# Performance work log

Measured on AMD Instinct MI355X. Metric: run time of the kernel, lower is better.

## Reference

```python
import jax, jax.numpy as jnp
import numpy as np

B, N, C, H, W = 2, 512, 32, 200, 200
THRESH = 0.05
# BEVCamera: x_range=y_range=(-1,1) -> FoV=2 meters; sh = H/FoVy = 100, sw = W/FoVx = 100
SH = H / 2.0
SW = W / 2.0
LOWPASS = 0.3        # 3DGS low-pass filter added to 2D cov diagonal
ALPHA_MIN = 1.0 / 255.0
ALPHA_MAX = 0.99


def setup_inputs() -> dict:
    key = jax.random.key(0)
    k1, k2, k3, k4 = jax.random.split(key, 4)
    features = jax.random.normal(k1, (B, N, C), dtype=jnp.float32)
    means3D = jax.random.uniform(k2, (B, N, 3), dtype=jnp.float32, minval=-1.0, maxval=1.0)
    # build PSD 3D covariances: Sigma = A A^T + eps*I, store 6 upper-tri entries
    A = 0.05 * jax.random.normal(k3, (B, N, 3, 3), dtype=jnp.float32)
    S = jnp.einsum('bnij,bnkj->bnik', A, A) + 1e-4 * jnp.eye(3, dtype=jnp.float32)
    cov3D = jnp.stack([S[..., 0, 0], S[..., 0, 1], S[..., 0, 2],
                       S[..., 1, 1], S[..., 1, 2], S[..., 2, 2]], axis=-1)
    opacities = jax.random.uniform(k4, (B, N, 1), dtype=jnp.float32)
    return {"features": features, "means3D": means3D, "cov3D": cov3D, "opacities": opacities}


def _render_one(features, means3D, cov3D, op):
    # features [N,C], means3D [N,3], cov3D [N,6] (xx,xy,xz,yy,yz,zz), op [N,1]
    dtype = features.dtype
    opac = op[:, 0]
    opac = jnp.where(opac > THRESH, opac, 0.0)  # masked-out gaussians contribute nothing
    # projmatrix: u = H/2 - sh*y (height), v = W/2 - sw*x (width)
    mu_u = H / 2.0 - SH * means3D[:, 1]
    mu_v = W / 2.0 - SW * means3D[:, 0]
    # 2D covariance from orthographic BEV projection J = [[0,-sh,0],[-sw,0,0]]
    Cuu = SH * SH * cov3D[:, 3] + LOWPASS
    Cvv = SW * SW * cov3D[:, 0] + LOWPASS
    Cuv = SH * SW * cov3D[:, 1]
    det = Cuu * Cvv - Cuv * Cuv
    valid = det > 0.0
    inv_det = jnp.where(valid, 1.0 / jnp.where(valid, det, 1.0), 0.0)
    Iuu = Cvv * inv_det
    Ivv = Cuu * inv_det
    Iuv = -Cuv * inv_det
    opac = jnp.where(valid, opac, 0.0)
    uu = jnp.arange(H, dtype=dtype)
    vv = jnp.arange(W, dtype=dtype)
    du = uu[None, :, None] - mu_u[:, None, None]   # [N,H,1]
    dv = vv[None, None, :] - mu_v[:, None, None]   # [N,1,W]
    power = (-0.5 * (Iuu[:, None, None] * du * du + Ivv[:, None, None] * dv * dv)
             - Iuv[:, None, None] * du * dv)       # [N,H,W]
    alpha = jnp.minimum(ALPHA_MAX, opac[:, None, None] * jnp.exp(jnp.minimum(power, 0.0)))
    alpha = jnp.where((power > 0.0) | (alpha < ALPHA_MIN), 0.0, alpha)
    # front-to-back alpha compositing in gaussian index order (all depths are 0 -> stable sort)
    logt = jnp.log1p(-alpha)                       # [N,H,W]
    T = jnp.exp(jnp.cumsum(logt, axis=0) - logt)   # exclusive transmittance
    w = T * alpha                                  # [N,H,W]
    return jnp.einsum('nhw,nc->chw', w, features)  # bg color is zeros


def reference(features, means3D, cov3D, opacities):
    bev = jax.vmap(_render_one)(features, means3D, cov3D, opacities)  # [B,C,H,W]
    num_gaussians = (opacities[..., 0] > THRESH).astype(jnp.float32).sum(axis=-1).mean()
    return bev, num_gaussians
```

## Files before the change

kernel.cpp:

```cpp
#include <hip/hip_runtime.h>
#include <math.h>

#define B_ 2
#define N_ 512
#define C_ 32
#define H_ 200
#define W_ 200
#define HW_ (H_*W_)
#define THRESH_ 0.05f
#define OUT_BEV (B_*C_*H_*W_)
#define NSEG 4
#define TILES_PER_B 625
#define LOG2E 1.4426950408889634f
#define LN2   0.6931471805599453f

typedef float v2f __attribute__((ext_vector_type(2)));

__device__ __forceinline__ float rlane(float x, int l) {
    return __int_as_float(__builtin_amdgcn_readlane(__float_as_int(x), l));
}

__device__ __forceinline__ void pcompute(
    const float* __restrict__ m3, const float* __restrict__ cv,
    const float* __restrict__ opc, int i,
    float& mu_u, float& mu_v, float& a2, float& b2, float& c2,
    float& opo, float& thr2, float& inv2a, float& inv2b)
{
    float x  = m3[i*3 + 0];
    float y  = m3[i*3 + 1];
    float c0 = cv[i*6 + 0];
    float c1 = cv[i*6 + 1];
    float c3 = cv[i*6 + 3];
    float op = opc[i];
    mu_u = 100.0f - 100.0f * y;
    mu_v = 100.0f - 100.0f * x;
    float Cuu = 10000.0f * c3 + 0.3f;
    float Cvv = 10000.0f * c0 + 0.3f;
    float Cuv = 10000.0f * c1;
    float det = Cuu * Cvv - Cuv * Cuv;
    bool valid = det > 0.0f;
    float opac = (op > THRESH_) ? op : 0.0f;
    if (!valid) opac = 0.0f;
    float inv_det = valid ? (1.0f / det) : 0.0f;
    a2 = -0.5f * LOG2E * (Cvv * inv_det);
    b2 = -0.5f * LOG2E * (Cuu * inv_det);
    c2 =  LOG2E * (Cuv * inv_det);
    opo = opac;
    if (opac > 0.0f) {
        thr2 = -log2f(255.0f * opac);
        inv2a = 1.0f / (2.0f * a2);
        inv2b = 1.0f / (2.0f * b2);
    } else {
        thr2 = 3.0e38f;
        inv2a = 0.0f;
        inv2b = 0.0f;
    }
}

__device__ __forceinline__ float edge_max_u(float a2, float b2, float c2,
                                            float due, float dvlo, float dvhi,
                                            float inv2b) {
    float dvs = fminf(fmaxf(-c2 * due * inv2b, dvlo), dvhi);
    return fmaf(a2 * due, due, fmaf(b2 * dvs, dvs, c2 * (due * dvs)));
}
__device__ __forceinline__ float edge_max_v(float a2, float b2, float c2,
                                            float dve, float dulo, float duhi,
                                            float inv2a) {
    float dus = fminf(fmaxf(-c2 * dve * inv2a, dulo), duhi);
    return fmaf(a2 * dus, dus, fmaf(b2 * dve, dve, c2 * (dus * dve)));
}

#define OVTEST(P, ovname)                                                     \
    bool ovname;                                                              \
    {                                                                         \
        float dulo = tu0 - P##_mu_u, duhi = tu1 - P##_mu_u;                   \
        float dvlo = tv0 - P##_mu_v, dvhi = tv1 - P##_mu_v;                   \
        bool inside = (dulo <= 0.0f) & (duhi >= 0.0f) &                       \
                      (dvlo <= 0.0f) & (dvhi >= 0.0f);                        \
        float e0 = edge_max_u(P##_a, P##_b, P##_c, dulo, dvlo, dvhi, P##_i2b);\
        float e1 = edge_max_u(P##_a, P##_b, P##_c, duhi, dvlo, dvhi, P##_i2b);\
        float e2 = edge_max_v(P##_a, P##_b, P##_c, dvlo, dulo, duhi, P##_i2a);\
        float e3 = edge_max_v(P##_a, P##_b, P##_c, dvhi, dulo, duhi, P##_i2a);\
        float mx = fmaxf(fmaxf(e0, e1), fmaxf(e2, e3));                       \
        ovname = (P##_op > 0.0f) && (inside || (mx >= P##_th));               \
    }

#define WALK(mask, P, base_n)                                                \
    while (mask) {                                                           \
        int j0 = __builtin_ctzll(mask); mask &= mask - 1;                    \
        bool two = (mask != 0ull);                                           \
        int j1 = two ? __builtin_ctzll(mask) : j0;                           \
        if (two) mask &= mask - 1;                                           \
        float mu_u0 = rlane(P##_mu_u, j0), mu_v0 = rlane(P##_mu_v, j0);      \
        float a0 = rlane(P##_a, j0), b0 = rlane(P##_b, j0);                  \
        float c0 = rlane(P##_c, j0), op0 = rlane(P##_op, j0);                \
        float th0 = rlane(P##_th, j0);                                       \
        float mu_u1 = rlane(P##_mu_u, j1), mu_v1 = rlane(P##_mu_v, j1);      \
        float a1 = rlane(P##_a, j1), b1 = rlane(P##_b, j1);                  \
        float c1 = rlane(P##_c, j1), op1 = rlane(P##_op, j1);                \
        float th1 = rlane(P##_th, j1);                                       \
        const v2f* f0 = (const v2f*)(featB + (size_t)((base_n) + j0) * C_);  \
        const v2f* f1 = (const v2f*)(featB + (size_t)((base_n) + j1) * C_);  \
        float du0 = u - mu_u0, dv0 = v - mu_v0;                              \
        float pw0 = fmaf(a0 * du0, du0, fmaf(b0 * dv0, dv0, c0 * (du0 * dv0))); \
        bool hit0 = (pw0 <= 0.0f) && (pw0 >= th0);                           \
        float al0 = hit0 ? fminf(0.99f, op0 * exp2f(pw0)) : 0.0f;            \
        float du1 = u - mu_u1, dv1 = v - mu_v1;                              \
        float pw1 = fmaf(a1 * du1, du1, fmaf(b1 * dv1, dv1, c1 * (du1 * dv1))); \
        bool hit1 = two && (pw1 <= 0.0f) && (pw1 >= th1);                    \
        float al1 = hit1 ? fminf(0.99f, op1 * exp2f(pw1)) : 0.0f;            \
        if (__any(hit0 | hit1)) {                                            \
            float w0 = T * al0;                                              \
            float Tm = T * (1.0f - al0);                                     \
            float w1 = Tm * al1;                                             \
            T = Tm * (1.0f - al1);                                           \
            v2f w0v = {w0, w0}, w1v = {w1, w1};                              \
            _Pragma("unroll")                                                \
            for (int i = 0; i < 16; ++i)                                     \
                acc2[i] = __builtin_elementwise_fma(w1v, f1[i],              \
                          __builtin_elementwise_fma(w0v, f0[i], acc2[i]));   \
        }                                                                    \
    }

__global__ __launch_bounds__(256, 5) void render_kernel(
    const float* __restrict__ features,
    const float* __restrict__ means3D,
    const float* __restrict__ cov3D,
    const float* __restrict__ opacities,
    float* __restrict__ out)
{
    __shared__ float s_T[NSEG][64];
    __shared__ unsigned int s_pk[NSEG * 16 * 64];

    int blk = blockIdx.x;
    int tid = threadIdx.x;

    if (blk == B_ * TILES_PER_B) {
        int cnt = ((opacities[tid]       > THRESH_) ? 1 : 0)
                + ((opacities[tid + 256] > THRESH_) ? 1 : 0)
                + ((opacities[tid + 512] > THRESH_) ? 1 : 0)
                + ((opacities[tid + 768] > THRESH_) ? 1 : 0);
        for (int off = 32; off > 0; off >>= 1) cnt += __shfl_down(cnt, off);
        int* s_red = (int*)s_T;
        if ((tid & 63) == 0) s_red[tid >> 6] = cnt;
        __syncthreads();
        if (tid == 0)
            out[OUT_BEV] = (float)(s_red[0] + s_red[1] + s_red[2] + s_red[3]) * 0.5f;
        return;
    }

    int b = blk & 1;
    int i = blk >> 1;
    int s = (int)sqrtf((float)i);
    int r = (s + 1) >> 1;
    int tu, tv;
    if (r == 0) {
        tu = 12; tv = 12;
    } else {
        int base = (2 * r - 1) * (2 * r - 1);
        int p  = i - base;
        int tr = 2 * r;
        int side = p / tr;
        int off  = p - side * tr;
        if      (side == 0) { tu = 12 - r + off; tv = 12 - r; }
        else if (side == 1) { tu = 12 + r;       tv = 12 - r + off; }
        else if (side == 2) { tu = 12 + r - off; tv = 12 + r; }
        else                { tu = 12 - r;       tv = 12 + r - off; }
    }

    int wave = __builtin_amdgcn_readfirstlane(tid >> 6);
    int lane = tid & 63;

    float tu0 = (float)(tu * 8), tu1 = tu0 + 7.0f;
    float tv0 = (float)(tv * 8), tv1 = tv0 + 7.0f;

    float A_mu_u, A_mu_v, A_a, A_b, A_c, A_op, A_th, A_i2a, A_i2b;
    float B_mu_u, B_mu_v, B_a, B_b, B_c, B_op, B_th, B_i2a, B_i2b;
    int i0 = b * N_ + wave * 128 + lane;
    pcompute(means3D, cov3D, opacities, i0,
             A_mu_u, A_mu_v, A_a, A_b, A_c, A_op, A_th, A_i2a, A_i2b);
    pcompute(means3D, cov3D, opacities, i0 + 64,
             B_mu_u, B_mu_v, B_a, B_b, B_c, B_op, B_th, B_i2a, B_i2b);

    OVTEST(A, ovA)
    OVTEST(B, ovB)
    unsigned long long m0 = __ballot(ovA);
    unsigned long long m1 = __ballot(ovB);

    int uu = tu * 8 + (lane >> 3);
    int vv = tv * 8 + (lane & 7);
    float u = (float)uu, v = (float)vv;

    float T = 1.0f;
    v2f acc2[16];
#pragma unroll
    for (int i2 = 0; i2 < 16; ++i2) acc2[i2] = (v2f){0.0f, 0.0f};
    const float* featB = features + (size_t)b * (N_ * C_);

    WALK(m0, A, wave * 128)
    WALK(m1, B, wave * 128 + 64)

    s_T[wave][lane] = T;
#pragma unroll
    for (int i2 = 0; i2 < 16; ++i2) {
        unsigned int rr;
        asm("v_cvt_pk_bf16_f32 %0, %1, %2"
            : "=v"(rr) : "v"(acc2[i2].x), "v"(acc2[i2].y));
        s_pk[(wave * 16 + i2) * 64 + lane] = rr;
    }
    __syncthreads();

    float t0g = s_T[0][lane], t1g = s_T[1][lane], t2g = s_T[2][lane];
    float Wg[NSEG];
    Wg[0] = 1.0f;
    Wg[1] = t0g;
    Wg[2] = t0g * t1g;
    Wg[3] = Wg[2] * t2g;

    size_t obase = (size_t)b * C_ * HW_ + (size_t)(tu * 8) * W_ + (size_t)(tv * 8);
    size_t opix  = (size_t)(lane >> 3) * W_ + (lane & 7);
#pragma unroll
    for (int q = 0; q < 4; ++q) {
        int pr = wave * 4 + q;
        float vlo = 0.0f, vhi = 0.0f;
#pragma unroll
        for (int g = 0; g < NSEG; ++g) {
            unsigned int rr = s_pk[(g * 16 + pr) * 64 + lane];
            float flo = __uint_as_float(rr << 16);
            float fhi = __uint_as_float(rr & 0xffff0000u);
            vlo = fmaf(Wg[g], flo, vlo);
            vhi = fmaf(Wg[g], fhi, vhi);
        }
        out[obase + (size_t)(2 * pr)     * HW_ + opix] = vlo;
        out[obase + (size_t)(2 * pr + 1) * HW_ + opix] = vhi;
    }
}

extern "C" void kernel_launch(void* const* d_in, const int* in_sizes, int n_in,
                              void* d_out, int out_size, void* d_ws, size_t ws_size,
                              hipStream_t stream) {
    const float* features  = (const float*)d_in[0];
    const float* means3D   = (const float*)d_in[1];
    const float* cov3D     = (const float*)d_in[2];
    const float* opacities = (const float*)d_in[3];
    float* out = (float*)d_out;
    render_kernel<<<B_ * TILES_PER_B + 1, 256, 0, stream>>>(
        features, means3D, cov3D, opacities, out);
}
```

Baseline: 16.50 us.

## Walk both 64-gaussian halves in parallel with independent transmittance chains

Replaces the two sequential walks over hit masks A and B with one loop that advances both masks together. Each half keeps its own transmittance and accumulator, and the results are combined at the end as accA + TA*accB. This breaks the serial dependency between the halves and makes the feature pointers wave-uniform, which should give the scheduler more independent work per iteration. In exchange it doubles the accumulator registers, which could reduce occupancy. It also drops the __any skip, so FMAs run on iterations where no lane hits, and the shorter mask is padded with idle iterations.

```diff
diff --git a/kernel.cpp b/kernel.cpp
--- a/kernel.cpp
+++ b/kernel.cpp
@@ -85,43 +85,6 @@
         ovname = (P##_op > 0.0f) && (inside || (mx >= P##_th));               \
     }
 
-#define WALK(mask, P, base_n)                                                \
-    while (mask) {                                                           \
-        int j0 = __builtin_ctzll(mask); mask &= mask - 1;                    \
-        bool two = (mask != 0ull);                                           \
-        int j1 = two ? __builtin_ctzll(mask) : j0;                           \
-        if (two) mask &= mask - 1;                                           \
-        float mu_u0 = rlane(P##_mu_u, j0), mu_v0 = rlane(P##_mu_v, j0);      \
-        float a0 = rlane(P##_a, j0), b0 = rlane(P##_b, j0);                  \
-        float c0 = rlane(P##_c, j0), op0 = rlane(P##_op, j0);                \
-        float th0 = rlane(P##_th, j0);                                       \
-        float mu_u1 = rlane(P##_mu_u, j1), mu_v1 = rlane(P##_mu_v, j1);      \
-        float a1 = rlane(P##_a, j1), b1 = rlane(P##_b, j1);                  \
-        float c1 = rlane(P##_c, j1), op1 = rlane(P##_op, j1);                \
-        float th1 = rlane(P##_th, j1);                                       \
-        const v2f* f0 = (const v2f*)(featB + (size_t)((base_n) + j0) * C_);  \
-        const v2f* f1 = (const v2f*)(featB + (size_t)((base_n) + j1) * C_);  \
-        float du0 = u - mu_u0, dv0 = v - mu_v0;                              \
-        float pw0 = fmaf(a0 * du0, du0, fmaf(b0 * dv0, dv0, c0 * (du0 * dv0))); \
-        bool hit0 = (pw0 <= 0.0f) && (pw0 >= th0);                           \
-        float al0 = hit0 ? fminf(0.99f, op0 * exp2f(pw0)) : 0.0f;            \
-        float du1 = u - mu_u1, dv1 = v - mu_v1;                              \
-        float pw1 = fmaf(a1 * du1, du1, fmaf(b1 * dv1, dv1, c1 * (du1 * dv1))); \
-        bool hit1 = two && (pw1 <= 0.0f) && (pw1 >= th1);                    \
-        float al1 = hit1 ? fminf(0.99f, op1 * exp2f(pw1)) : 0.0f;            \
-        if (__any(hit0 | hit1)) {                                            \
-            float w0 = T * al0;                                              \
-            float Tm = T * (1.0f - al0);                                     \
-            float w1 = Tm * al1;                                             \
-            T = Tm * (1.0f - al1);                                           \
-            v2f w0v = {w0, w0}, w1v = {w1, w1};                              \
-            _Pragma("unroll")                                                \
-            for (int i = 0; i < 16; ++i)                                     \
-                acc2[i] = __builtin_elementwise_fma(w1v, f1[i],              \
-                          __builtin_elementwise_fma(w0v, f0[i], acc2[i]));   \
-        }                                                                    \
-    }
-
 __global__ __launch_bounds__(256, 5) void render_kernel(
     const float* __restrict__ features,
     const float* __restrict__ means3D,
@@ -191,14 +154,70 @@
     int vv = tv * 8 + (lane & 7);
     float u = (float)uu, v = (float)vv;
 
-    float T = 1.0f;
+    const float* featB = features + (size_t)b * (N_ * C_);
+    int baseA = wave * 128;
+    int baseB = wave * 128 + 64;
+
+    int nhA = __builtin_amdgcn_readfirstlane(__popcll(m0));
+    int nhB = __builtin_amdgcn_readfirstlane(__popcll(m1));
+    int nmax = nhA > nhB ? nhA : nhB;
+
+    float TA = 1.0f, TB = 1.0f;
+    v2f accA[16], accB[16];
+#pragma unroll
+    for (int i2 = 0; i2 < 16; ++i2) { accA[i2] = (v2f){0.f,0.f}; accB[i2] = (v2f){0.f,0.f}; }
+    unsigned long long wAm = m0, wBm = m1;
+
+    for (int k = 0; k < nmax; ++k) {
+        bool liveA = (k < nhA);
+        bool liveB = (k < nhB);
+        unsigned long long mA = wAm ? wAm : 1ull;
+        unsigned long long mB = wBm ? wBm : 1ull;
+        int jA = __builtin_ctzll(mA);
+        int jB = __builtin_ctzll(mB);
+        wAm &= wAm - 1;
+        wBm &= wBm - 1;
+
+        float mu_u0 = rlane(A_mu_u, jA), mu_v0 = rlane(A_mu_v, jA);
+        float a0 = rlane(A_a, jA), b0 = rlane(A_b, jA);
+        float c0 = rlane(A_c, jA), op0 = rlane(A_op, jA), th0 = rlane(A_th, jA);
+        float mu_u1 = rlane(B_mu_u, jB), mu_v1 = rlane(B_mu_v, jB);
+        float a1 = rlane(B_a, jB), b1 = rlane(B_b, jB);
+        float c1 = rlane(B_c, jB), op1 = rlane(B_op, jB), th1 = rlane(B_th, jB);
+
+        int nA = __builtin_amdgcn_readfirstlane(baseA + jA);
+        int nB = __builtin_amdgcn_readfirstlane(baseB + jB);
+        const v2f* f0 = (const v2f*)(featB + (size_t)nA * C_);
+        const v2f* f1 = (const v2f*)(featB + (size_t)nB * C_);
+
+        float du0 = u - mu_u0, dv0 = v - mu_v0;
+        float pw0 = fmaf(a0 * du0, du0, fmaf(b0 * dv0, dv0, c0 * (du0 * dv0)));
+        bool hit0 = liveA && (pw0 <= 0.0f) && (pw0 >= th0);
+        float al0 = hit0 ? fminf(0.99f, op0 * exp2f(pw0)) : 0.0f;
+        float w0 = TA * al0;
+        TA *= (1.0f - al0);
+
+        float du1 = u - mu_u1, dv1 = v - mu_v1;
+        float pw1 = fmaf(a1 * du1, du1, fmaf(b1 * dv1, dv1, c1 * (du1 * dv1)));
+        bool hit1 = liveB && (pw1 <= 0.0f) && (pw1 >= th1);
+        float al1 = hit1 ? fminf(0.99f, op1 * exp2f(pw1)) : 0.0f;
+        float w1 = TB * al1;
+        TB *= (1.0f - al1);
+
+        v2f w0v = {w0, w0}, w1v = {w1, w1};
+#pragma unroll
+        for (int i2 = 0; i2 < 16; ++i2) {
+            accA[i2] = __builtin_elementwise_fma(w0v, f0[i2], accA[i2]);
+            accB[i2] = __builtin_elementwise_fma(w1v, f1[i2], accB[i2]);
+        }
+    }
+
+    float T = TA * TB;
+    v2f tav = {TA, TA};
     v2f acc2[16];
 #pragma unroll
-    for (int i2 = 0; i2 < 16; ++i2) acc2[i2] = (v2f){0.0f, 0.0f};
-    const float* featB = features + (size_t)b * (N_ * C_);
-
-    WALK(m0, A, wave * 128)
-    WALK(m1, B, wave * 128 + 64)
+    for (int i2 = 0; i2 < 16; ++i2)
+        acc2[i2] = __builtin_elementwise_fma(tav, accB[i2], accA[i2]);
 
     s_T[wave][lane] = T;
 #pragma unroll
```

New measurement: 18.33 us. +11.1%, slower.
